# Optimization experiments

Hardware: AMD Instinct MI355X
Metric: run time of the kernel (lower is better)

## Reference

```python
import jax, jax.numpy as jnp
import numpy as np

EPS = 1e-5

def _bn(x, g, b, m, v):
    # eval-mode BatchNorm1d over channel dim of [B, C, T]
    scale = g / jnp.sqrt(v + EPS)
    return (x - m[:, None]) * scale[:, None] + b[:, None]

def _conv3(x, w, b):
    # [B, W, T] conv with kernel [W, W, 3], padding=1
    y = jax.lax.conv_general_dilated(x, w, (1,), [(1, 1)],
                                     dimension_numbers=('NCH', 'OIH', 'NCH'))
    return y + b[None, :, None]

def setup_inputs() -> dict:
    key = jax.random.key(0)
    ks = iter(jax.random.split(key, 32))
    def n(shape, s=0.05):
        return jax.random.normal(next(ks), shape, jnp.float32) * s
    def u(shape):
        return jax.random.uniform(next(ks), shape, jnp.float32, 0.5, 1.5)
    B, T, C, S, W = 128, 4096, 125, 5, 25
    return dict(
        low_freq=jax.random.normal(next(ks), (B, 10, T), jnp.float32),
        w1=n((S, W, 2)), b1=n((S, W)),
        w3=n((S - 1, W, W, 3)), b3=n((S - 1, W)),
        bn_g=jnp.ones((S, W)), bn_b=jnp.zeros((S, W)), bn_m=n((S, W)), bn_v=u((S, W)),
        gw1=n((C // 4, C)), gb1=n((C // 4,)),          # gating Linear(125, 31)
        gw2=n((S, C // 4)), gb2=n((S,)),               # gating Linear(31, 5)
        id_w=n((C, 10)), id_b=n((C,)),                 # identity_proj Conv1d(10,125,1)
        pf_w=n((C, C)), pf_b=n((C,)),                  # proj_final Conv1d(125,125,1)
        fbn_g=jnp.ones((C,)), fbn_b=jnp.zeros((C,)), fbn_m=n((C,)), fbn_v=u((C,)),
        ln_g=jnp.ones((C,)), ln_b=jnp.zeros((C,)),
        fc1_w=n((64, C)), fc1_b=n((64,)),
        fc2_w=n((2, 64)), fc2_b=n((2,)),
    )

def reference(low_freq, w1, b1, w3, b3, bn_g, bn_b, bn_m, bn_v,
              gw1, gb1, gw2, gb2, id_w, id_b, pf_w, pf_b,
              fbn_g, fbn_b, fbn_m, fbn_v, ln_g, ln_b,
              fc1_w, fc1_b, fc2_w, fc2_b):
    S = w1.shape[0]
    B, _, T = low_freq.shape
    identity = jnp.einsum('bct,oc->bot', low_freq, id_w) + id_b[None, :, None]
    chunks = low_freq.reshape(B, S, 2, T)              # torch.chunk over 10 channels
    # all 1x1 convs at once: [S, B, W, T]
    xs = jnp.einsum('bsct,swc->sbwt', chunks, w1) + b1[:, None, :, None]
    y = [None] * S
    y[S - 1] = jax.nn.relu(_bn(xs[S - 1], bn_g[S - 1], bn_b[S - 1], bn_m[S - 1], bn_v[S - 1]))
    for i in range(S - 2, -1, -1):                     # sequential Res2Net recursion
        yi = _conv3(xs[i] + y[i + 1], w3[i], b3[i])
        y[i] = jax.nn.relu(_bn(yi, bn_g[i], bn_b[i], bn_m[i], bn_v[i]))
    ms = jnp.concatenate(y, axis=1)                    # [B, 125, T]
    avg = jnp.mean(ms, axis=-1)                        # [B, 125]
    gate = jax.nn.sigmoid(jax.nn.relu(avg @ gw1.T + gb1) @ gw2.T + gb2)  # [B, S]
    yw = jnp.stack(y, axis=1) * gate[:, :, None, None] # [B, S, W, T]
    gated = yw.reshape(B, -1, T)
    proj = jnp.einsum('bct,oc->bot', gated, pf_w) + pf_b[None, :, None]
    out = jax.nn.relu(_bn(proj + identity, fbn_g, fbn_b, fbn_m, fbn_v))
    pooled = jnp.mean(out, axis=-1)                    # GAP -> [B, 125]
    mu = jnp.mean(pooled, axis=-1, keepdims=True)
    var = jnp.var(pooled, axis=-1, keepdims=True)
    normed = (pooled - mu) / jnp.sqrt(var + EPS) * ln_g + ln_b
    h = normed @ fc1_w.T + fc1_b
    h = jnp.where(h > 0, h, 0.2 * h)                   # LeakyReLU(0.2); dropout = identity (eval)
    return h @ fc2_w.T + fc2_b                         # [B, 2]
```

## Files before the change

kernel.cpp:

```cpp
#include <hip/hip_runtime.h>
#include <stdint.h>

typedef unsigned short u16;
typedef unsigned int   u32;
using short8 = __attribute__((ext_vector_type(8))) short;
using f32x4  = __attribute__((ext_vector_type(4))) float;

__device__ __forceinline__ u16 f2bf(float f){
  u32 u = __builtin_bit_cast(u32, f);
  u = u + 0x7fffu + ((u >> 16) & 1u);
  return (u16)(u >> 16);
}
__device__ __forceinline__ u32 packbf2(float a, float b){
  u32 ua = __builtin_bit_cast(u32, a) + 0x8000u;
  u32 ub = __builtin_bit_cast(u32, b) + 0x8000u;
  return (ua >> 16) | (ub & 0xffff0000u);
}

__global__ void prep_kernel(const float* __restrict__ w3, u16* __restrict__ convA){
  int idx = blockIdx.x*256 + threadIdx.x;
  if (idx >= 4*2*3*64*8) return;
  int j = idx & 7, l = (idx>>3) & 63, frag = idx >> 9;
  int tap = frag % 3, mt = (frag/3) & 1, lay = frag/6;
  int m = mt*16 + (l & 15), k = (l>>4)*8 + j;
  float v = 0.f;
  if (m < 25 && k < 25) v = w3[((lay*25 + m)*25 + k)*3 + tap];
  convA[idx] = f2bf(v);
}

template<int PASS, int CT>
__global__ __launch_bounds__(256)
void pass_kernel(const float* __restrict__ lfg,
                 const float* __restrict__ w1g, const float* __restrict__ b1g,
                 const float* __restrict__ b3g,
                 const float* __restrict__ bng, const float* __restrict__ bnb,
                 const float* __restrict__ bnm, const float* __restrict__ bnv,
                 const u16* __restrict__ convA, const u16* __restrict__ Ab,
                 const float* __restrict__ pfb, const float* __restrict__ idb,
                 const float* __restrict__ fbg, const float* __restrict__ fbb,
                 const float* __restrict__ fbm, const float* __restrict__ fbv,
                 float* __restrict__ outpart)
{
  constexpr int IS   = (CT-2)*16;
  constexpr int LFC  = 4*IS + 32;
  constexpr int CZ   = 16*CT + 2;
  constexpr int NBLK = 4096/(4*IS);

  __shared__ __align__(16) u16 zws[4][CZ*40];
  __shared__ __align__(16) u16 yTs[(PASS==2)?4:1][(PASS==2)?(32*40):8];
  __shared__ float lfs[10][LFC];
  __shared__ float abnA[5][32], cbnA[5][32], w1A[5][32][2], b1A[5][32];
  __shared__ float accC[(PASS==1)?160:4];
  __shared__ float pooled[(PASS==2)?128:4];
  __shared__ float AfS[(PASS==2)?128:4], BfS[(PASS==2)?128:4];

  const int tid  = threadIdx.x;
  const int lane = tid & 63, wv = tid >> 6;
  const int q = lane >> 4, c16 = lane & 15;
  const int b = blockIdx.y, blk = blockIdx.x;
  const int stripe = blk*4 + wv;
  const int tbase  = stripe*IS - 16;
  const int colB   = blk*(4*IS) - 16;

  for (int x = tid; x < 4*CZ*20; x += 256) ((u32*)zws)[x] = 0u;
  if constexpr (PASS==2){
    for (int x = tid; x < 4*32*20; x += 256) ((u32*)yTs)[x] = 0u;
  }
  for (int x = tid; x < 10*LFC; x += 256){
    int ch = x / LFC, u = x - ch*LFC;
    int t = colB + u;
    lfs[ch][u] = ((unsigned)t < 4096u) ? lfg[(b*10 + ch)*4096 + t] : 0.f;
  }
  if (tid < 160){
    int i = tid >> 5, ch = tid & 31;
    float a=0.f, c=0.f, w0=0.f, w1v=0.f, bb=0.f;
    if (ch < 25){
      float g = bng[i*25+ch], be = bnb[i*25+ch], m = bnm[i*25+ch], v = bnv[i*25+ch];
      a = g * rsqrtf(v + 1e-5f);
      c = (i==4) ? (be - m*a) : ((b3g[i*25+ch] - m)*a + be);
      w0 = w1g[(i*25+ch)*2+0]; w1v = w1g[(i*25+ch)*2+1]; bb = b1g[i*25+ch];
    }
    abnA[i][ch]=a; cbnA[i][ch]=c; w1A[i][ch][0]=w0; w1A[i][ch][1]=w1v; b1A[i][ch]=bb;
  }
  if constexpr (PASS==1){ if (tid < 160) accC[tid] = 0.f; }
  if constexpr (PASS==2){
    if (tid < 128){
      pooled[tid] = 0.f;
      float fs=0.f, fsh=0.f;
      if (tid < 125){
        fs  = fbg[tid]*rsqrtf(fbv[tid]+1e-5f);
        fsh = (pfb[tid]+idb[tid]-fbm[tid])*fs + fbb[tid];
      }
      AfS[tid]=fs; BfS[tid]=fsh;
    }
  }
  __syncthreads();

  u16* z  = zws[wv];
  u16* yt = yTs[(PASS==2)?wv:0];
  const int lfo = wv*IS;

  f32x4 pacc[2][8];
  if constexpr (PASS==2){
    #pragma unroll
    for (int n2 = 0; n2 < 2; ++n2)
      #pragma unroll
      for (int m2 = 0; m2 < 8; ++m2) pacc[n2][m2] = (f32x4){0.f,0.f,0.f,0.f};
  }

  {
    float s4[8];
    #pragma unroll
    for (int m2 = 0; m2 < 8; ++m2) s4[m2] = 0.f;
    #pragma unroll
    for (int ct = 0; ct < CT; ++ct){
      const int lc = 16*ct + c16;
      const int t  = tbase + lc;
      const bool tok   = (unsigned)t < 4096u;
      const bool inter = (ct >= 1) && (ct <= CT-2);
      const float lf6 = lfs[6][lfo+lc], lf7 = lfs[7][lfo+lc];
      const float lf8 = lfs[8][lfo+lc], lf9 = lfs[9][lfo+lc];
      #pragma unroll
      for (int mt = 0; mt < 2; ++mt){
        float zv[4], yv[4];
        #pragma unroll
        for (int r = 0; r < 4; ++r){
          const int ch = mt*16 + 4*q + r;
          float xs4 = b1A[4][ch] + w1A[4][ch][0]*lf8 + w1A[4][ch][1]*lf9;
          float y4  = fmaxf(abnA[4][ch]*xs4 + cbnA[4][ch], 0.f);
          float xs3 = b1A[3][ch] + w1A[3][ch][0]*lf6 + w1A[3][ch][1]*lf7;
          zv[r] = tok ? (xs3 + y4) : 0.f;
          yv[r] = y4;
          if (PASS==1 && inter) s4[mt*4+r] += y4;
        }
        uint2 wz; wz.x = packbf2(zv[0], zv[1]); wz.y = packbf2(zv[2], zv[3]);
        *(uint2*)&z[(lc+1)*40 + mt*16 + 4*q] = wz;
        if (PASS==2 && inter){
          uint2 wy; wy.x = packbf2(yv[0], yv[1]); wy.y = packbf2(yv[2], yv[3]);
          *(uint2*)&yt[(lc-16)*40 + mt*16 + 4*q] = wy;
        }
      }
    }
    if constexpr (PASS==1){
      #pragma unroll
      for (int m2 = 0; m2 < 8; ++m2){
        float v = s4[m2];
        v += __shfl_xor(v,1); v += __shfl_xor(v,2); v += __shfl_xor(v,4); v += __shfl_xor(v,8);
        if (c16 == 0){
          int ch = (m2>>2)*16 + 4*q + (m2&3);
          if (ch < 25) atomicAdd(&accC[4*32+ch], v);
        }
      }
    }
  }

  if constexpr (PASS==2){
    {
      short8 Am[8];
      #pragma unroll
      for (int m2 = 0; m2 < 8; ++m2)
        Am[m2] = *(const short8*)(Ab + b*24576 + ((4*8+m2)*64 + lane)*8);
      #pragma unroll
      for (int n2 = 0; n2 < 2; ++n2){
        const short8 Bm = *(const short8*)&yt[(n2*16 + c16)*40 + 8*q];
        #pragma unroll
        for (int m2 = 0; m2 < 8; ++m2)
          pacc[n2][m2] = __builtin_amdgcn_mfma_f32_16x16x32_bf16(Am[m2], Bm, pacc[n2][m2], 0,0,0);
      }
    }
    {
      short8 Am[8];
      #pragma unroll
      for (int m2 = 0; m2 < 8; ++m2)
        Am[m2] = *(const short8*)(Ab + b*24576 + ((5*8+m2)*64 + lane)*8);
      #pragma unroll
      for (int n2 = 0; n2 < 2; ++n2){
        short8 Bm;
        #pragma unroll
        for (int j = 0; j < 8; ++j){
          int k = 8*q + j;
          float v = (k < 10) ? lfs[k][lfo + 16 + n2*16 + c16] : 0.f;
          Bm[j] = (short)f2bf(v);
        }
        #pragma unroll
        for (int m2 = 0; m2 < 8; ++m2)
          pacc[n2][m2] = __builtin_amdgcn_mfma_f32_16x16x32_bf16(Am[m2], Bm, pacc[n2][m2], 0,0,0);
      }
    }
  }

  for (int i = 3; i >= 0; --i){
    short8 Ac0[3], Ac1[3];
    #pragma unroll
    for (int tp = 0; tp < 3; ++tp){
      Ac0[tp] = *(const short8*)(convA + (((i*2+0)*3+tp)*64 + lane)*8);
      Ac1[tp] = *(const short8*)(convA + (((i*2+1)*3+tp)*64 + lane)*8);
    }
    float ysum[8];
    #pragma unroll
    for (int m2 = 0; m2 < 8; ++m2) ysum[m2] = 0.f;

    short8 fA[3], fB[3];
    {
      const u16* p = z + c16*40 + 8*q;
      fA[0] = *(const short8*)(p);
      fA[1] = *(const short8*)(p + 40);
      fA[2] = *(const short8*)(p + 80);
    }
    #pragma unroll
    for (int ct = 0; ct < CT; ++ct){
      short8* cur = (ct & 1) ? fB : fA;
      short8* nxt = (ct & 1) ? fA : fB;
      if (ct < CT-1){
        const u16* p = z + (16*(ct+1) + c16)*40 + 8*q;
        nxt[0] = *(const short8*)(p);
        nxt[1] = *(const short8*)(p + 40);
        nxt[2] = *(const short8*)(p + 80);
      }
      __builtin_amdgcn_sched_barrier(0);
      f32x4 a0 = {0.f,0.f,0.f,0.f}, a1 = {0.f,0.f,0.f,0.f};
      #pragma unroll
      for (int tp = 0; tp < 3; ++tp){
        a0 = __builtin_amdgcn_mfma_f32_16x16x32_bf16(Ac0[tp], cur[tp], a0, 0,0,0);
        a1 = __builtin_amdgcn_mfma_f32_16x16x32_bf16(Ac1[tp], cur[tp], a1, 0,0,0);
      }
      const int lc = 16*ct + c16;
      const int t  = tbase + lc;
      const bool tok   = (unsigned)t < 4096u;
      const bool inter = (ct >= 1) && (ct <= CT-2);
      float lfa = 0.f, lfb = 0.f;
      if (i > 0){ lfa = lfs[2*i-2][lfo+lc]; lfb = lfs[2*i-1][lfo+lc]; }
      #pragma unroll
      for (int mt = 0; mt < 2; ++mt){
        float yv[4], zv[4];
        #pragma unroll
        for (int r = 0; r < 4; ++r){
          const int ch = mt*16 + 4*q + r;
          const float av = mt ? a1[r] : a0[r];
          float y = fmaxf(av*abnA[i][ch] + cbnA[i][ch], 0.f);
          yv[r] = y;
          if (PASS==1 && inter) ysum[mt*4+r] += y;
          if (i > 0) zv[r] = tok ? (y + b1A[i-1][ch] + w1A[i-1][ch][0]*lfa
                                      + w1A[i-1][ch][1]*lfb) : 0.f;
        }
        if (PASS==2 && inter){
          uint2 wy; wy.x = packbf2(yv[0], yv[1]); wy.y = packbf2(yv[2], yv[3]);
          *(uint2*)&yt[(lc-16)*40 + mt*16 + 4*q] = wy;
        }
        if (i > 0){
          uint2 wz; wz.x = packbf2(zv[0], zv[1]); wz.y = packbf2(zv[2], zv[3]);
          *(uint2*)&z[(lc+1)*40 + mt*16 + 4*q] = wz;
        }
      }
    }
    if constexpr (PASS==1){
      #pragma unroll
      for (int m2 = 0; m2 < 8; ++m2){
        float v = ysum[m2];
        v += __shfl_xor(v,1); v += __shfl_xor(v,2); v += __shfl_xor(v,4); v += __shfl_xor(v,8);
        if (c16 == 0){
          int ch = (m2>>2)*16 + 4*q + (m2&3);
          if (ch < 25) atomicAdd(&accC[i*32+ch], v);
        }
      }
    }
    if constexpr (PASS==2){
      short8 Am[8];
      #pragma unroll
      for (int m2 = 0; m2 < 8; ++m2)
        Am[m2] = *(const short8*)(Ab + b*24576 + ((i*8+m2)*64 + lane)*8);
      #pragma unroll
      for (int n2 = 0; n2 < 2; ++n2){
        const short8 Bm = *(const short8*)&yt[(n2*16 + c16)*40 + 8*q];
        #pragma unroll
        for (int m2 = 0; m2 < 8; ++m2)
          pacc[n2][m2] = __builtin_amdgcn_mfma_f32_16x16x32_bf16(Am[m2], Bm, pacc[n2][m2], 0,0,0);
      }
    }
  }

  if constexpr (PASS==1){
    __syncthreads();
    if (tid < 160) outpart[(b*NBLK + blk)*160 + tid] = accC[tid];
  }
  if constexpr (PASS==2){
    #pragma unroll
    for (int m2 = 0; m2 < 8; ++m2){
      float p0=0.f,p1=0.f,p2=0.f,p3=0.f;
      const int chb = m2*16 + 4*q;
      #pragma unroll
      for (int n2 = 0; n2 < 2; ++n2){
        p0 += fmaxf(pacc[n2][m2][0]*AfS[chb+0] + BfS[chb+0], 0.f);
        p1 += fmaxf(pacc[n2][m2][1]*AfS[chb+1] + BfS[chb+1], 0.f);
        p2 += fmaxf(pacc[n2][m2][2]*AfS[chb+2] + BfS[chb+2], 0.f);
        p3 += fmaxf(pacc[n2][m2][3]*AfS[chb+3] + BfS[chb+3], 0.f);
      }
      p0 += __shfl_xor(p0,1); p0 += __shfl_xor(p0,2); p0 += __shfl_xor(p0,4); p0 += __shfl_xor(p0,8);
      p1 += __shfl_xor(p1,1); p1 += __shfl_xor(p1,2); p1 += __shfl_xor(p1,4); p1 += __shfl_xor(p1,8);
      p2 += __shfl_xor(p2,1); p2 += __shfl_xor(p2,2); p2 += __shfl_xor(p2,4); p2 += __shfl_xor(p2,8);
      p3 += __shfl_xor(p3,1); p3 += __shfl_xor(p3,2); p3 += __shfl_xor(p3,4); p3 += __shfl_xor(p3,8);
      if (c16 == 0){
        atomicAdd(&pooled[chb+0], p0); atomicAdd(&pooled[chb+1], p1);
        atomicAdd(&pooled[chb+2], p2); atomicAdd(&pooled[chb+3], p3);
      }
    }
    __syncthreads();
    if (tid < 128) outpart[(b*NBLK + blk)*128 + tid] = pooled[tid];
  }
}

__global__ void gate_kernel(const float* __restrict__ partialC,
                            const float* __restrict__ gw1, const float* __restrict__ gb1,
                            const float* __restrict__ gw2, const float* __restrict__ gb2,
                            const float* __restrict__ pf_w, const float* __restrict__ id_w,
                            u16* __restrict__ Ab)
{
  int b = blockIdx.x, tid = threadIdx.x;
  __shared__ float avg[125], h1[31], g[6];
  if (tid < 160){
    float s = 0.f;
    for (int k = 0; k < 16; ++k) s += partialC[(b*16+k)*160 + tid];
    int sc = tid >> 5, ch = tid & 31;
    if (ch < 25) avg[sc*25+ch] = s * (1.f/4096.f);
  }
  __syncthreads();
  if (tid < 31){
    float s = gb1[tid];
    for (int c = 0; c < 125; ++c) s += avg[c] * gw1[tid*125 + c];
    h1[tid] = fmaxf(s, 0.f);
  }
  __syncthreads();
  if (tid < 5){
    float s = gb2[tid];
    for (int j = 0; j < 31; ++j) s += h1[j] * gw2[tid*31 + j];
    g[tid] = 1.f / (1.f + expf(-s));
  }
  if (tid == 5) g[5] = 1.f;
  __syncthreads();
  for (int idx = tid; idx < 24576; idx += 256){
    int j = idx & 7, l = (idx>>3) & 63, mt = (idx>>9) & 7, kt = idx >> 12;
    int m = mt*16 + (l & 15), k = (l>>4)*8 + j;
    float v = 0.f;
    if (m < 125){
      if (kt < 5){ if (k < 25) v = pf_w[m*125 + kt*25 + k] * g[kt]; }
      else       { if (k < 10) v = id_w[m*10 + k]; }
    }
    Ab[b*24576 + idx] = f2bf(v);
  }
}

__global__ void final_kernel(const float* __restrict__ pooledpart,
                             const float* __restrict__ ln_g, const float* __restrict__ ln_b,
                             const float* __restrict__ fc1_w, const float* __restrict__ fc1_b,
                             const float* __restrict__ fc2_w, const float* __restrict__ fc2_b,
                             float* __restrict__ out)
{
  int b = blockIdx.x, tid = threadIdx.x;
  __shared__ float pl[125], nr[125], hh[64], st[2];
  for (int c = tid; c < 125; c += 64){
    float s = 0.f;
    for (int k = 0; k < 32; ++k) s += pooledpart[(b*32+k)*128 + c];
    pl[c] = s * (1.f/4096.f);
  }
  __syncthreads();
  if (tid == 0){
    float mu = 0.f;
    for (int c = 0; c < 125; ++c) mu += pl[c];
    mu /= 125.f;
    float va = 0.f;
    for (int c = 0; c < 125; ++c){ float d = pl[c] - mu; va += d*d; }
    va /= 125.f;
    st[0] = mu; st[1] = rsqrtf(va + 1e-5f);
  }
  __syncthreads();
  for (int c = tid; c < 125; c += 64)
    nr[c] = (pl[c] - st[0]) * st[1] * ln_g[c] + ln_b[c];
  __syncthreads();
  {
    float s = fc1_b[tid];
    for (int c = 0; c < 125; ++c) s += nr[c] * fc1_w[tid*125 + c];
    hh[tid] = (s > 0.f) ? s : 0.2f * s;
  }
  __syncthreads();
  if (tid < 2){
    float s = fc2_b[tid];
    for (int j = 0; j < 64; ++j) s += hh[j] * fc2_w[tid*64 + j];
    out[b*2 + tid] = s;
  }
}

extern "C" void kernel_launch(void* const* d_in, const int* in_sizes, int n_in,
                              void* d_out, int out_size, void* d_ws, size_t ws_size,
                              hipStream_t stream)
{
  const float* lf    = (const float*)d_in[0];
  const float* w1    = (const float*)d_in[1];
  const float* b1    = (const float*)d_in[2];
  const float* w3    = (const float*)d_in[3];
  const float* b3    = (const float*)d_in[4];
  const float* bn_g  = (const float*)d_in[5];
  const float* bn_b  = (const float*)d_in[6];
  const float* bn_m  = (const float*)d_in[7];
  const float* bn_v  = (const float*)d_in[8];
  const float* gw1   = (const float*)d_in[9];
  const float* gb1   = (const float*)d_in[10];
  const float* gw2   = (const float*)d_in[11];
  const float* gb2   = (const float*)d_in[12];
  const float* id_w  = (const float*)d_in[13];
  const float* id_b  = (const float*)d_in[14];
  const float* pf_w  = (const float*)d_in[15];
  const float* pf_b  = (const float*)d_in[16];
  const float* fbn_g = (const float*)d_in[17];
  const float* fbn_b = (const float*)d_in[18];
  const float* fbn_m = (const float*)d_in[19];
  const float* fbn_v = (const float*)d_in[20];
  const float* ln_g  = (const float*)d_in[21];
  const float* ln_b  = (const float*)d_in[22];
  const float* fc1_w = (const float*)d_in[23];
  const float* fc1_b = (const float*)d_in[24];
  const float* fc2_w = (const float*)d_in[25];
  const float* fc2_b = (const float*)d_in[26];

  char* ws = (char*)d_ws;
  float* partialC   = (float*)ws;
  float* pooledpart = (float*)(ws + 1310720);
  u16*   Ab         = (u16*)(ws + 1310720 + 2097152);
  u16*   convA      = (u16*)(ws + 1310720 + 2097152 + 6291456);

  prep_kernel<<<48, 256, 0, stream>>>(w3, convA);
  dim3 g1(16, 128), g2(32, 128);
  pass_kernel<1,6><<<g1, 256, 0, stream>>>(lf, w1, b1, b3, bn_g, bn_b, bn_m, bn_v,
      convA, Ab, pf_b, id_b, fbn_g, fbn_b, fbn_m, fbn_v, partialC);
  gate_kernel<<<128, 256, 0, stream>>>(partialC, gw1, gb1, gw2, gb2, pf_w, id_w, Ab);
  pass_kernel<2,4><<<g2, 256, 0, stream>>>(lf, w1, b1, b3, bn_g, bn_b, bn_m, bn_v,
      convA, Ab, pf_b, id_b, fbn_g, fbn_b, fbn_m, fbn_v, pooledpart);
  final_kernel<<<128, 64, 0, stream>>>(pooledpart, ln_g, ln_b, fc1_w, fc1_b,
      fc2_w, fc2_b, (float*)d_out);
}
```

Measured before the change: 434.9 us.

## Fold 1x1 convs and BN scale into conv3 weights, drop lf and yT shared buffers

Folds the BN scale and the per-scale 1x1 conv (bias and two input-channel weights) into the conv3 MFMA weights. The conv input tile now carries the previous y plus a constant-one channel and the two raw input channels, so the elementwise z computation collapses to a bias-add and ReLU. The lf and yT shared tiles are removed: inputs are read straight from global into registers and the z tile is reused as the B operand of the projection. Pooled partials are now written per wave with no shared atomics, and launch bounds request higher occupancy. The cost is more global traffic, a larger partial buffer for the final kernel to reduce, and bf16 rounding of the raw inputs inside the conv.

```diff
diff --git a/kernel.cpp b/kernel.cpp
--- a/kernel.cpp
+++ b/kernel.cpp
@@ -17,19 +17,40 @@
   return (ua >> 16) | (ub & 0xffff0000u);
 }
 
-__global__ void prep_kernel(const float* __restrict__ w3, u16* __restrict__ convA){
+__global__ void prep_kernel(const float* __restrict__ w3,
+                            const float* __restrict__ w1,
+                            const float* __restrict__ b1,
+                            const float* __restrict__ bng,
+                            const float* __restrict__ bnv,
+                            u16* __restrict__ convA)
+{
   int idx = blockIdx.x*256 + threadIdx.x;
   if (idx >= 4*2*3*64*8) return;
   int j = idx & 7, l = (idx>>3) & 63, frag = idx >> 9;
   int tap = frag % 3, mt = (frag/3) & 1, lay = frag/6;
-  int m = mt*16 + (l & 15), k = (l>>4)*8 + j;
+  int m = mt*16 + (l & 15);
+  int k = (l>>4)*8 + j;
   float v = 0.f;
-  if (m < 25 && k < 25) v = w3[((lay*25 + m)*25 + k)*3 + tap];
+  if (m < 25){
+    float a = bng[lay*25+m] * rsqrtf(bnv[lay*25+m] + 1e-5f);
+    if (k < 25){
+      v = a * w3[((lay*25+m)*25 + k)*3 + tap];
+    } else if (k == 25){
+      float s = 0.f;
+      for (int c = 0; c < 25; ++c) s += w3[((lay*25+m)*25+c)*3+tap] * b1[lay*25+c];
+      v = a * s;
+    } else if (k <= 27){
+      int e = k - 26;
+      float s = 0.f;
+      for (int c = 0; c < 25; ++c) s += w3[((lay*25+m)*25+c)*3+tap] * w1[(lay*25+c)*2+e];
+      v = a * s;
+    }
+  }
   convA[idx] = f2bf(v);
 }
 
 template<int PASS, int CT>
-__global__ __launch_bounds__(256)
+__global__ __launch_bounds__(256, (PASS==1) ? 4 : 2)
 void pass_kernel(const float* __restrict__ lfg,
                  const float* __restrict__ w1g, const float* __restrict__ b1g,
                  const float* __restrict__ b3g,
@@ -42,17 +63,14 @@
                  float* __restrict__ outpart)
 {
   constexpr int IS   = (CT-2)*16;
-  constexpr int LFC  = 4*IS + 32;
   constexpr int CZ   = 16*CT + 2;
   constexpr int NBLK = 4096/(4*IS);
 
   __shared__ __align__(16) u16 zws[4][CZ*40];
-  __shared__ __align__(16) u16 yTs[(PASS==2)?4:1][(PASS==2)?(32*40):8];
-  __shared__ float lfs[10][LFC];
-  __shared__ float abnA[5][32], cbnA[5][32], w1A[5][32][2], b1A[5][32];
+  __shared__ __align__(16) float cAs[4][32];
+  __shared__ __align__(16) float w4as[32], w4bs[32], c4s[32];
   __shared__ float accC[(PASS==1)?160:4];
-  __shared__ float pooled[(PASS==2)?128:4];
-  __shared__ float AfS[(PASS==2)?128:4], BfS[(PASS==2)?128:4];
+  __shared__ __align__(16) float AfS[(PASS==2)?128:4], BfS[(PASS==2)?128:4];
 
   const int tid  = threadIdx.x;
   const int lane = tid & 63, wv = tid >> 6;
@@ -60,32 +78,35 @@
   const int b = blockIdx.y, blk = blockIdx.x;
   const int stripe = blk*4 + wv;
   const int tbase  = stripe*IS - 16;
-  const int colB   = blk*(4*IS) - 16;
 
   for (int x = tid; x < 4*CZ*20; x += 256) ((u32*)zws)[x] = 0u;
-  if constexpr (PASS==2){
-    for (int x = tid; x < 4*32*20; x += 256) ((u32*)yTs)[x] = 0u;
-  }
-  for (int x = tid; x < 10*LFC; x += 256){
-    int ch = x / LFC, u = x - ch*LFC;
-    int t = colB + u;
-    lfs[ch][u] = ((unsigned)t < 4096u) ? lfg[(b*10 + ch)*4096 + t] : 0.f;
-  }
-  if (tid < 160){
+  __syncthreads();
+  for (int x = tid; x < 4*CZ; x += 256){
+    int w = x / CZ, cz = x - w*CZ;
+    int t = (blk*4 + w)*IS - 16 + cz - 1;
+    zws[w][cz*40 + 25] = ((unsigned)t < 4096u) ? (u16)0x3F80 : (u16)0;
+  }
+  if (tid < 128){
     int i = tid >> 5, ch = tid & 31;
-    float a=0.f, c=0.f, w0=0.f, w1v=0.f, bb=0.f;
+    float cc = 0.f;
     if (ch < 25){
-      float g = bng[i*25+ch], be = bnb[i*25+ch], m = bnm[i*25+ch], v = bnv[i*25+ch];
-      a = g * rsqrtf(v + 1e-5f);
-      c = (i==4) ? (be - m*a) : ((b3g[i*25+ch] - m)*a + be);
-      w0 = w1g[(i*25+ch)*2+0]; w1v = w1g[(i*25+ch)*2+1]; bb = b1g[i*25+ch];
-    }
-    abnA[i][ch]=a; cbnA[i][ch]=c; w1A[i][ch][0]=w0; w1A[i][ch][1]=w1v; b1A[i][ch]=bb;
+      float a = bng[i*25+ch]*rsqrtf(bnv[i*25+ch]+1e-5f);
+      cc = (b3g[i*25+ch] - bnm[i*25+ch])*a + bnb[i*25+ch];
+    }
+    cAs[i][ch] = cc;
+  } else if (tid < 160){
+    int ch = tid - 128;
+    float wa=0.f, wb=0.f, cf=0.f;
+    if (ch < 25){
+      float a = bng[100+ch]*rsqrtf(bnv[100+ch]+1e-5f);
+      wa = a*w1g[(100+ch)*2+0]; wb = a*w1g[(100+ch)*2+1];
+      cf = a*b1g[100+ch] + (bnb[100+ch] - bnm[100+ch]*a);
+    }
+    w4as[ch]=wa; w4bs[ch]=wb; c4s[ch]=cf;
   }
   if constexpr (PASS==1){ if (tid < 160) accC[tid] = 0.f; }
   if constexpr (PASS==2){
     if (tid < 128){
-      pooled[tid] = 0.f;
       float fs=0.f, fsh=0.f;
       if (tid < 125){
         fs  = fbg[tid]*rsqrtf(fbv[tid]+1e-5f);
@@ -96,58 +117,72 @@
   }
   __syncthreads();
 
-  u16* z  = zws[wv];
-  u16* yt = yTs[(PASS==2)?wv:0];
-  const int lfo = wv*IS;
+  u16* z = zws[wv];
 
   f32x4 pacc[2][8];
   if constexpr (PASS==2){
     #pragma unroll
-    for (int n2 = 0; n2 < 2; ++n2)
-      #pragma unroll
-      for (int m2 = 0; m2 < 8; ++m2) pacc[n2][m2] = (f32x4){0.f,0.f,0.f,0.f};
+    for (int n2=0;n2<2;++n2)
+      #pragma unroll
+      for (int m2=0;m2<8;++m2) pacc[n2][m2] = (f32x4){0.f,0.f,0.f,0.f};
   }
 
   {
+    float l8[CT], l9[CT], r0[CT], r1[CT];
+    #pragma unroll
+    for (int ct=0; ct<CT; ++ct){
+      int t = tbase + 16*ct + c16;
+      bool tk = (unsigned)t < 4096u;
+      l8[ct] = tk ? lfg[(b*10+8)*4096 + t] : 0.f;
+      l9[ct] = tk ? lfg[(b*10+9)*4096 + t] : 0.f;
+      r0[ct] = 0.f; r1[ct] = 0.f;
+      if (lane < 16 && tk){
+        r0[ct] = lfg[(b*10+6)*4096 + t];
+        r1[ct] = lfg[(b*10+7)*4096 + t];
+      }
+    }
+    const f32x4 wa0 = *(const f32x4*)&w4as[4*q];
+    const f32x4 wa1 = *(const f32x4*)&w4as[16+4*q];
+    const f32x4 wb0 = *(const f32x4*)&w4bs[4*q];
+    const f32x4 wb1 = *(const f32x4*)&w4bs[16+4*q];
+    const f32x4 cf0 = *(const f32x4*)&c4s[4*q];
+    const f32x4 cf1 = *(const f32x4*)&c4s[16+4*q];
     float s4[8];
     #pragma unroll
-    for (int m2 = 0; m2 < 8; ++m2) s4[m2] = 0.f;
-    #pragma unroll
-    for (int ct = 0; ct < CT; ++ct){
+    for (int e=0;e<8;++e) s4[e] = 0.f;
+    #pragma unroll
+    for (int ct=0; ct<CT; ++ct){
       const int lc = 16*ct + c16;
       const int t  = tbase + lc;
       const bool tok   = (unsigned)t < 4096u;
       const bool inter = (ct >= 1) && (ct <= CT-2);
-      const float lf6 = lfs[6][lfo+lc], lf7 = lfs[7][lfo+lc];
-      const float lf8 = lfs[8][lfo+lc], lf9 = lfs[9][lfo+lc];
-      #pragma unroll
-      for (int mt = 0; mt < 2; ++mt){
-        float zv[4], yv[4];
-        #pragma unroll
-        for (int r = 0; r < 4; ++r){
-          const int ch = mt*16 + 4*q + r;
-          float xs4 = b1A[4][ch] + w1A[4][ch][0]*lf8 + w1A[4][ch][1]*lf9;
-          float y4  = fmaxf(abnA[4][ch]*xs4 + cbnA[4][ch], 0.f);
-          float xs3 = b1A[3][ch] + w1A[3][ch][0]*lf6 + w1A[3][ch][1]*lf7;
-          zv[r] = tok ? (xs3 + y4) : 0.f;
-          yv[r] = y4;
-          if (PASS==1 && inter) s4[mt*4+r] += y4;
-        }
-        uint2 wz; wz.x = packbf2(zv[0], zv[1]); wz.y = packbf2(zv[2], zv[3]);
-        *(uint2*)&z[(lc+1)*40 + mt*16 + 4*q] = wz;
-        if (PASS==2 && inter){
-          uint2 wy; wy.x = packbf2(yv[0], yv[1]); wy.y = packbf2(yv[2], yv[3]);
-          *(uint2*)&yt[(lc-16)*40 + mt*16 + 4*q] = wy;
-        }
-      }
+      float y0[4], y1[4];
+      #pragma unroll
+      for (int r=0;r<4;++r){
+        float a = fmaxf(wa0[r]*l8[ct] + wb0[r]*l9[ct] + cf0[r], 0.f);
+        float c = fmaxf(wa1[r]*l8[ct] + wb1[r]*l9[ct] + cf1[r], 0.f);
+        y0[r] = tok ? a : 0.f;
+        y1[r] = tok ? c : 0.f;
+        if (PASS==1 && inter){ s4[r] += y0[r]; s4[4+r] += y1[r]; }
+      }
+      uint2 w0; w0.x = packbf2(y0[0],y0[1]); w0.y = packbf2(y0[2],y0[3]);
+      *(uint2*)&z[(lc+1)*40 + 4*q] = w0;
+      if (q < 2){
+        uint2 w1_; w1_.x = packbf2(y1[0],y1[1]); w1_.y = packbf2(y1[2],y1[3]);
+        *(uint2*)&z[(lc+1)*40 + 16 + 4*q] = w1_;
+      } else if (q == 2){
+        z[(lc+1)*40 + 24] = f2bf(y1[0]);
+      }
+      if (lane < 16)
+        *(u32*)&z[(16*ct+lane+1)*40 + 26] = packbf2(r0[ct], r1[ct]);
     }
     if constexpr (PASS==1){
       #pragma unroll
-      for (int m2 = 0; m2 < 8; ++m2){
-        float v = s4[m2];
+      for (int e=0;e<8;++e){
+        float v = s4[e];
         v += __shfl_xor(v,1); v += __shfl_xor(v,2); v += __shfl_xor(v,4); v += __shfl_xor(v,8);
         if (c16 == 0){
-          int ch = (m2>>2)*16 + 4*q + (m2&3);
+          int ch = (e>>2)*16 + 4*q + (e&3);
           if (ch < 25) atomicAdd(&accC[4*32+ch], v);
         }
       }
@@ -158,33 +193,36 @@
     {
       short8 Am[8];
       #pragma unroll
-      for (int m2 = 0; m2 < 8; ++m2)
+      for (int m2=0;m2<8;++m2)
         Am[m2] = *(const short8*)(Ab + b*24576 + ((4*8+m2)*64 + lane)*8);
       #pragma unroll
-      for (int n2 = 0; n2 < 2; ++n2){
-        const short8 Bm = *(const short8*)&yt[(n2*16 + c16)*40 + 8*q];
+      for (int n2=0;n2<2;++n2){
+        const short8 Bm = *(const short8*)&z[(17+16*n2+c16)*40 + 8*q];
         #pragma unroll
-        for (int m2 = 0; m2 < 8; ++m2)
-          pacc[n2][m2] = __builtin_amdgcn_mfma_f32_16x16x32_bf16(Am[m2], Bm, pacc[n2][m2], 0,0,0);
+        for (int m2=0;m2<8;++m2)
+          pacc[n2][m2] = __builtin_amdgcn_mfma_f32_16x16x32_bf16(Am[m2], Bm, pacc[n2][m2],0,0,0);
       }
     }
     {
       short8 Am[8];
       #pragma unroll
-      for (int m2 = 0; m2 < 8; ++m2)
+      for (int m2=0;m2<8;++m2)
         Am[m2] = *(const short8*)(Ab + b*24576 + ((5*8+m2)*64 + lane)*8);
       #pragma unroll
-      for (int n2 = 0; n2 < 2; ++n2){
-        short8 Bm;
+      for (int n2=0;n2<2;++n2){
+        const int t = tbase + 16 + 16*n2 + c16;
+        u32 bw[4];
         #pragma unroll
-        for (int j = 0; j < 8; ++j){
-          int k = 8*q + j;
-          float v = (k < 10) ? lfs[k][lfo + 16 + n2*16 + c16] : 0.f;
-          Bm[j] = (short)f2bf(v);
+        for (int p=0;p<4;++p){
+          int k0 = 8*q + 2*p;
+          float v0 = (k0   < 10) ? lfg[(b*10+k0  )*4096 + t] : 0.f;
+          float v1 = (k0+1 < 10) ? lfg[(b*10+k0+1)*4096 + t] : 0.f;
+          bw[p] = packbf2(v0, v1);
         }
+        const short8 Bm = __builtin_bit_cast(short8, bw);
         #pragma unroll
-        for (int m2 = 0; m2 < 8; ++m2)
-          pacc[n2][m2] = __builtin_amdgcn_mfma_f32_16x16x32_bf16(Am[m2], Bm, pacc[n2][m2], 0,0,0);
+        for (int m2=0;m2<8;++m2)
+          pacc[n2][m2] = __builtin_amdgcn_mfma_f32_16x16x32_bf16(Am[m2], Bm, pacc[n2][m2],0,0,0);
       }
     }
   }
@@ -192,35 +230,60 @@
   for (int i = 3; i >= 0; --i){
     short8 Ac0[3], Ac1[3];
     #pragma unroll
-    for (int tp = 0; tp < 3; ++tp){
+    for (int tp=0;tp<3;++tp){
       Ac0[tp] = *(const short8*)(convA + (((i*2+0)*3+tp)*64 + lane)*8);
       Ac1[tp] = *(const short8*)(convA + (((i*2+1)*3+tp)*64 + lane)*8);
     }
+    const f32x4 cc0 = *(const f32x4*)&cAs[i][4*q];
+    const f32x4 cc1 = *(const f32x4*)&cAs[i][16+4*q];
+    short8 Ag[8];
+    if constexpr (PASS==2){
+      #pragma unroll
+      for (int m2=0;m2<8;++m2)
+        Ag[m2] = *(const short8*)(Ab + b*24576 + ((i*8+m2)*64 + lane)*8);
+    }
+    float r0[CT], r1[CT];
+    #pragma unroll
+    for (int ct=0;ct<CT;++ct){ r0[ct]=0.f; r1[ct]=0.f; }
+    if (i > 0 && lane < 16){
+      #pragma unroll
+      for (int ct=0;ct<CT;++ct){
+        int t = tbase + 16*ct + lane;
+        if ((unsigned)t < 4096u){
+          r0[ct] = lfg[(b*10 + 2*i-2)*4096 + t];
+          r1[ct] = lfg[(b*10 + 2*i-1)*4096 + t];
+        }
+      }
+    }
     float ysum[8];
     #pragma unroll
-    for (int m2 = 0; m2 < 8; ++m2) ysum[m2] = 0.f;
-
-    short8 fA[3], fB[3];
+    for (int e=0;e<8;++e) ysum[e] = 0.f;
+
+    short8 F0[3], F1[3], F2[3];
     {
       const u16* p = z + c16*40 + 8*q;
-      fA[0] = *(const short8*)(p);
-      fA[1] = *(const short8*)(p + 40);
-      fA[2] = *(const short8*)(p + 80);
-    }
-    #pragma unroll
-    for (int ct = 0; ct < CT; ++ct){
-      short8* cur = (ct & 1) ? fB : fA;
-      short8* nxt = (ct & 1) ? fA : fB;
-      if (ct < CT-1){
-        const u16* p = z + (16*(ct+1) + c16)*40 + 8*q;
-        nxt[0] = *(const short8*)(p);
-        nxt[1] = *(const short8*)(p + 40);
-        nxt[2] = *(const short8*)(p + 80);
+      F0[0] = *(const short8*)(p);
+      F0[1] = *(const short8*)(p + 40);
+      F0[2] = *(const short8*)(p + 80);
+      const u16* p1 = z + (16 + c16)*40 + 8*q;
+      F1[0] = *(const short8*)(p1);
+      F1[1] = *(const short8*)(p1 + 40);
+      F1[2] = *(const short8*)(p1 + 80);
+    }
+    #pragma unroll
+    for (int ct=0; ct<CT; ++ct){
+      short8* cur = (ct%3==0) ? F0 : ((ct%3==1) ? F1 : F2);
+      short8* nx2 = (ct%3==0) ? F2 : ((ct%3==1) ? F0 : F1);
+      if (ct < CT-2){
+        const u16* p = z + (16*(ct+2) + c16)*40 + 8*q;
+        nx2[0] = *(const short8*)(p);
+        nx2[1] = *(const short8*)(p + 40);
+        nx2[2] = *(const short8*)(p + 80);
       }
       __builtin_amdgcn_sched_barrier(0);
       f32x4 a0 = {0.f,0.f,0.f,0.f}, a1 = {0.f,0.f,0.f,0.f};
       #pragma unroll
-      for (int tp = 0; tp < 3; ++tp){
+      for (int tp=0;tp<3;++tp){
         a0 = __builtin_amdgcn_mfma_f32_16x16x32_bf16(Ac0[tp], cur[tp], a0, 0,0,0);
         a1 = __builtin_amdgcn_mfma_f32_16x16x32_bf16(Ac1[tp], cur[tp], a1, 0,0,0);
       }
@@ -228,53 +291,46 @@
       const int t  = tbase + lc;
       const bool tok   = (unsigned)t < 4096u;
       const bool inter = (ct >= 1) && (ct <= CT-2);
-      float lfa = 0.f, lfb = 0.f;
-      if (i > 0){ lfa = lfs[2*i-2][lfo+lc]; lfb = lfs[2*i-1][lfo+lc]; }
-      #pragma unroll
-      for (int mt = 0; mt < 2; ++mt){
-        float yv[4], zv[4];
-        #pragma unroll
-        for (int r = 0; r < 4; ++r){
-          const int ch = mt*16 + 4*q + r;
-          const float av = mt ? a1[r] : a0[r];
-          float y = fmaxf(av*abnA[i][ch] + cbnA[i][ch], 0.f);
-          yv[r] = y;
-          if (PASS==1 && inter) ysum[mt*4+r] += y;
-          if (i > 0) zv[r] = tok ? (y + b1A[i-1][ch] + w1A[i-1][ch][0]*lfa
-                                      + w1A[i-1][ch][1]*lfb) : 0.f;
+      float y0[4], y1[4];
+      #pragma unroll
+      for (int r=0;r<4;++r){
+        float u0 = fmaxf(a0[r] + cc0[r], 0.f);
+        float u1 = fmaxf(a1[r] + cc1[r], 0.f);
+        y0[r] = tok ? u0 : 0.f;
+        y1[r] = tok ? u1 : 0.f;
+        if (PASS==1 && inter){ ysum[r] += y0[r]; ysum[4+r] += y1[r]; }
+      }
+      if (i > 0 || PASS==2){
+        uint2 w0; w0.x = packbf2(y0[0],y0[1]); w0.y = packbf2(y0[2],y0[3]);
+        *(uint2*)&z[(lc+1)*40 + 4*q] = w0;
+        if (q < 2){
+          uint2 w1_; w1_.x = packbf2(y1[0],y1[1]); w1_.y = packbf2(y1[2],y1[3]);
+          *(uint2*)&z[(lc+1)*40 + 16 + 4*q] = w1_;
+        } else if (q == 2){
+          z[(lc+1)*40 + 24] = f2bf(y1[0]);
         }
-        if (PASS==2 && inter){
-          uint2 wy; wy.x = packbf2(yv[0], yv[1]); wy.y = packbf2(yv[2], yv[3]);
-          *(uint2*)&yt[(lc-16)*40 + mt*16 + 4*q] = wy;
-        }
-        if (i > 0){
-          uint2 wz; wz.x = packbf2(zv[0], zv[1]); wz.y = packbf2(zv[2], zv[3]);
-          *(uint2*)&z[(lc+1)*40 + mt*16 + 4*q] = wz;
-        }
-      }
+      }
+      if (i > 0 && lane < 16)
+        *(u32*)&z[(16*ct+lane+1)*40 + 26] = packbf2(r0[ct], r1[ct]);
     }
     if constexpr (PASS==1){
       #pragma unroll
-      for (int m2 = 0; m2 < 8; ++m2){
-        float v = ysum[m2];
+      for (int e=0;e<8;++e){
+        float v = ysum[e];
         v += __shfl_xor(v,1); v += __shfl_xor(v,2); v += __shfl_xor(v,4); v += __shfl_xor(v,8);
         if (c16 == 0){
-          int ch = (m2>>2)*16 + 4*q + (m2&3);
+          int ch = (e>>2)*16 + 4*q + (e&3);
           if (ch < 25) atomicAdd(&accC[i*32+ch], v);
         }
       }
     }
     if constexpr (PASS==2){
-      short8 Am[8];
-      #pragma unroll
-      for (int m2 = 0; m2 < 8; ++m2)
-        Am[m2] = *(const short8*)(Ab + b*24576 + ((i*8+m2)*64 + lane)*8);
-      #pragma unroll
-      for (int n2 = 0; n2 < 2; ++n2){
-        const short8 Bm = *(const short8*)&yt[(n2*16 + c16)*40 + 8*q];
+      #pragma unroll
+      for (int n2=0;n2<2;++n2){
+        const short8 Bm = *(const short8*)&z[(17+16*n2+c16)*40 + 8*q];
         #pragma unroll
-        for (int m2 = 0; m2 < 8; ++m2)
-          pacc[n2][m2] = __builtin_amdgcn_mfma_f32_16x16x32_bf16(Am[m2], Bm, pacc[n2][m2], 0,0,0);
+        for (int m2=0;m2<8;++m2)
+          pacc[n2][m2] = __builtin_amdgcn_mfma_f32_16x16x32_bf16(Ag[m2], Bm, pacc[n2][m2],0,0,0);
       }
     }
   }
@@ -284,28 +340,25 @@
     if (tid < 160) outpart[(b*NBLK + blk)*160 + tid] = accC[tid];
   }
   if constexpr (PASS==2){
-    #pragma unroll
-    for (int m2 = 0; m2 < 8; ++m2){
-      float p0=0.f,p1=0.f,p2=0.f,p3=0.f;
-      const int chb = m2*16 + 4*q;
-      #pragma unroll
-      for (int n2 = 0; n2 < 2; ++n2){
-        p0 += fmaxf(pacc[n2][m2][0]*AfS[chb+0] + BfS[chb+0], 0.f);
-        p1 += fmaxf(pacc[n2][m2][1]*AfS[chb+1] + BfS[chb+1], 0.f);
-        p2 += fmaxf(pacc[n2][m2][2]*AfS[chb+2] + BfS[chb+2], 0.f);
-        p3 += fmaxf(pacc[n2][m2][3]*AfS[chb+3] + BfS[chb+3], 0.f);
-      }
-      p0 += __shfl_xor(p0,1); p0 += __shfl_xor(p0,2); p0 += __shfl_xor(p0,4); p0 += __shfl_xor(p0,8);
-      p1 += __shfl_xor(p1,1); p1 += __shfl_xor(p1,2); p1 += __shfl_xor(p1,4); p1 += __shfl_xor(p1,8);
-      p2 += __shfl_xor(p2,1); p2 += __shfl_xor(p2,2); p2 += __shfl_xor(p2,4); p2 += __shfl_xor(p2,8);
-      p3 += __shfl_xor(p3,1); p3 += __shfl_xor(p3,2); p3 += __shfl_xor(p3,4); p3 += __shfl_xor(p3,8);
-      if (c16 == 0){
-        atomicAdd(&pooled[chb+0], p0); atomicAdd(&pooled[chb+1], p1);
-        atomicAdd(&pooled[chb+2], p2); atomicAdd(&pooled[chb+3], p3);
-      }
-    }
-    __syncthreads();
-    if (tid < 128) outpart[(b*NBLK + blk)*128 + tid] = pooled[tid];
+    f32x4 ps[8];
+    #pragma unroll
+    for (int m2=0;m2<8;++m2){
+      const f32x4 af = *(const f32x4*)&AfS[m2*16+4*q];
+      const f32x4 bf = *(const f32x4*)&BfS[m2*16+4*q];
+      #pragma unroll
+      for (int r=0;r<4;++r){
+        float s = fmaxf(pacc[0][m2][r]*af[r] + bf[r], 0.f)
+                + fmaxf(pacc[1][m2][r]*af[r] + bf[r], 0.f);
+        s += __shfl_xor(s,1); s += __shfl_xor(s,2); s += __shfl_xor(s,4); s += __shfl_xor(s,8);
+        ps[m2][r] = s;
+      }
+    }
+    if (c16 == 0){
+      const int widx = (b*NBLK + blk)*4 + wv;
+      #pragma unroll
+      for (int m2=0;m2<8;++m2)
+        *(f32x4*)&outpart[widx*128 + m2*16 + 4*q] = ps[m2];
+    }
   }
 }
 
@@ -359,7 +412,7 @@
   __shared__ float pl[125], nr[125], hh[64], st[2];
   for (int c = tid; c < 125; c += 64){
     float s = 0.f;
-    for (int k = 0; k < 32; ++k) s += pooledpart[(b*32+k)*128 + c];
+    for (int k = 0; k < 128; ++k) s += pooledpart[(b*128+k)*128 + c];
     pl[c] = s * (1.f/4096.f);
   }
   __syncthreads();
@@ -424,16 +477,15 @@
   char* ws = (char*)d_ws;
   float* partialC   = (float*)ws;
   float* pooledpart = (float*)(ws + 1310720);
-  u16*   Ab         = (u16*)(ws + 1310720 + 2097152);
-  u16*   convA      = (u16*)(ws + 1310720 + 2097152 + 6291456);
-
-  prep_kernel<<<48, 256, 0, stream>>>(w3, convA);
-  dim3 g1(16, 128), g2(32, 128);
-  pass_kernel<1,6><<<g1, 256, 0, stream>>>(lf, w1, b1, b3, bn_g, bn_b, bn_m, bn_v,
-      convA, Ab, pf_b, id_b, fbn_g, fbn_b, fbn_m, fbn_v, partialC);
+  u16*   Ab         = (u16*)(ws + 1310720 + 8388608);
+  u16*   convA      = (u16*)(ws + 1310720 + 8388608 + 6291456);
+
+  prep_kernel<<<48, 256, 0, stream>>>(w3, w1, b1, bn_g, bn_v, convA);
+  pass_kernel<1,6><<<dim3(16,128), 256, 0, stream>>>(lf, w1, b1, b3, bn_g, bn_b,
+      bn_m, bn_v, convA, Ab, pf_b, id_b, fbn_g, fbn_b, fbn_m, fbn_v, partialC);
   gate_kernel<<<128, 256, 0, stream>>>(partialC, gw1, gb1, gw2, gb2, pf_w, id_w, Ab);
-  pass_kernel<2,4><<<g2, 256, 0, stream>>>(lf, w1, b1, b3, bn_g, bn_b, bn_m, bn_v,
-      convA, Ab, pf_b, id_b, fbn_g, fbn_b, fbn_m, fbn_v, pooledpart);
+  pass_kernel<2,4><<<dim3(32,128), 256, 0, stream>>>(lf, w1, b1, b3, bn_g, bn_b,
+      bn_m, bn_v, convA, Ab, pf_b, id_b, fbn_g, fbn_b, fbn_m, fbn_v, pooledpart);
   final_kernel<<<128, 64, 0, stream>>>(pooledpart, ln_g, ln_b, fc1_w, fc1_b,
       fc2_w, fc2_b, (float*)d_out);
 }
```

Measured after the change: 357.4 us. 1.22x faster.
